# Kernel tuning notes

Measured on AMD Instinct MI355X. Metric: run time of the kernel, lower is better.

The kernel has to match this reference:

```python
import jax, jax.numpy as jnp
import numpy as np

B = 1024      # batchsz
T = 80        # max_review_len
E = 100       # embedding_len
U = 256       # units
V = 10000     # total_words


def _lstm_cell(x, c, h, wf, bf, wi, bi, wc, bc, wo, bo):
    # Faithful to LSTMlayer.call: four separate concat+matmul+bias gates.
    hx = jnp.concatenate([h, x], axis=1)          # [B, U + sec_dim]
    gf = jax.nn.sigmoid(hx @ wf + bf)             # forget gate
    gi = jax.nn.sigmoid(hx @ wi + bi)             # input gate (gr / wr1)
    ct = jnp.tanh(hx @ wc + bc)                   # candidate (wr2)
    c_new = gf * c + gi * ct
    go = jax.nn.sigmoid(hx @ wo + bo)             # output gate
    h_new = go * jnp.tanh(c_new)
    return c_new, h_new


def setup_inputs() -> dict:
    key = jax.random.key(0)
    ks = jax.random.split(key, 21)
    inp = {"tokens": jax.random.randint(ks[0], (B, T), 0, V, dtype=jnp.int32)}
    inp["emb"] = jax.random.normal(ks[1], (V, E), dtype=jnp.float32) * 0.1
    # Layer 1: sec_dim = E; Layer 2: sec_dim = U. stddev=0.1 matches init_weights.
    names = ["wf1", "wi1", "wc1", "wo1", "wf2", "wi2", "wc2", "wo2"]
    dims = [U + E] * 4 + [U + U] * 4
    for i, (n, d) in enumerate(zip(names, dims)):
        inp[n] = jax.random.normal(ks[2 + i], (d, U), dtype=jnp.float32) * 0.1
        inp["b" + n[1:]] = jnp.zeros((U,), dtype=jnp.float32)
    inp["w_out"] = jax.random.normal(ks[10], (U, 1), dtype=jnp.float32) * 0.1
    inp["b_out"] = jnp.zeros((1,), dtype=jnp.float32)
    return inp


def reference(tokens, emb, wf1, bf1, wi1, bi1, wc1, bc1, wo1, bo1,
              wf2, bf2, wi2, bi2, wc2, bc2, wo2, bo2, w_out, b_out):
    x = emb[tokens]                               # [B, T, E]
    init = (jnp.zeros((B, U), x.dtype), jnp.zeros((B, U), x.dtype),
            jnp.zeros((B, U), x.dtype), jnp.zeros((B, U), x.dtype))

    def step(carry, xt):
        c1, h1, c2, h2 = carry
        c1, h1 = _lstm_cell(xt, c1, h1, wf1, bf1, wi1, bi1, wc1, bc1, wo1, bo1)
        c2, h2 = _lstm_cell(h1, c2, h2, wf2, bf2, wi2, bi2, wc2, bc2, wo2, bo2)
        return (c1, h1, c2, h2), None

    carry, _ = jax.lax.scan(step, init, jnp.swapaxes(x, 0, 1))  # scan over T
    h2_last = carry[3]                            # [B, U]
    return jax.nn.sigmoid(h2_last @ w_out + b_out)  # [B, 1]
```

## Files before the change

### kernel.cpp

```cpp
#include <hip/hip_runtime.h>

typedef unsigned short u16;
typedef unsigned int uint;

using f32x4 = __attribute__((ext_vector_type(4))) float;
using bf16x8 = __attribute__((ext_vector_type(8))) __bf16;
using u32x4 = __attribute__((ext_vector_type(4))) uint;

static __device__ __forceinline__ bf16x8 as_bf16x8(uint4 u) {
    union { uint4 a; bf16x8 b; } c; c.a = u; return c.b;
}
static __device__ __forceinline__ bf16x8 as_bf16x8v(u32x4 u) {
    union { u32x4 a; bf16x8 b; } c; c.a = u; return c.b;
}
static __device__ __forceinline__ float bf2f(u16 h) {
    union { uint u; float f; } c; c.u = ((uint)h) << 16; return c.f;
}
static __device__ __forceinline__ u16 f2bf(float f) {
    union { float f; uint u; } c; c.f = f;
    uint u = c.u;
    return (u16)((u + 0x7fffu + ((u >> 16) & 1u)) >> 16);
}
static __device__ __forceinline__ float fast_sigmoid(float x) {
    x = fminf(30.f, fmaxf(-30.f, x));
    return __builtin_amdgcn_rcpf(1.0f + __builtin_amdgcn_exp2f(x * -1.44269504f));
}
static __device__ __forceinline__ float fast_tanh(float x) {
    x = fminf(15.f, fmaxf(-15.f, x));
    return 1.0f - 2.0f * __builtin_amdgcn_rcpf(1.0f + __builtin_amdgcn_exp2f(x * 2.88539008f));
}

static __device__ __forceinline__ u32x4 load_b128_sc0(const u16* p) {
    u32x4 r;
    asm volatile("global_load_dwordx4 %0, %1, off sc0" : "=v"(r) : "v"(p) : "memory");
    return r;
}
static __device__ __forceinline__ void wait_vm0_fence_sched() {
    asm volatile("s_waitcnt vmcnt(0)" ::: "memory");
    __builtin_amdgcn_sched_barrier(0);
}

static __device__ __forceinline__ float vext(f32x4 v, int i) {
    float r = v[0];
    r = (i == 1) ? v[1] : r;
    r = (i == 2) ? v[2] : r;
    r = (i == 3) ? v[3] : r;
    return r;
}
static __device__ __forceinline__ float sel4(float a0, float a1, float a2, float a3, int i) {
    float r = a0;
    r = (i == 1) ? a1 : r;
    r = (i == 2) ? a2 : r;
    r = (i == 3) ? a3 : r;
    return r;
}

static __device__ __forceinline__ int detect_fp32(const uint* w, int nwords) {
    int hits = 0;
    for (int i = 0; i < nwords; ++i) { uint e = (w[i] >> 7) & 0xffu; hits += (e >= 0x80u); }
    return hits > (nwords >> 3);
}
static __device__ __forceinline__ u16 load_bf(const void* p, int i, int fp32) {
    return fp32 ? f2bf(((const float*)p)[i]) : ((const u16*)p)[i];
}

__global__ void pack_w(const void* wf, const void* wi, const void* wc, const void* wo,
                       const void* bbf, const void* bbi, const void* bbc, const void* bbo,
                       u16* __restrict__ wp, u16* __restrict__ bp, int K, int KSTEPS) {
    __shared__ int sfp;
    if (threadIdx.x == 0) sfp = detect_fp32((const uint*)wf, 256);
    __syncthreads();
    const int fp32 = sfp;
    int w = blockIdx.x / KSTEPS, ks = blockIdx.x % KSTEPS;
    int nt = threadIdx.x >> 6, lane = threadIdx.x & 63;
    int c16 = lane & 15, q = lane >> 4;
    int n = w * 64 + nt * 16 + c16;
    int u = n >> 2, g = n & 3;
    const void* W = (g == 0) ? wf : (g == 1) ? wi : (g == 2) ? wc : wo;
    union { u16 v[8]; uint4 u4; } tmp;
#pragma unroll
    for (int j = 0; j < 8; ++j) {
        int k = ks * 32 + q * 8 + j;
        tmp.v[j] = (k < K) ? load_bf(W, k * 256 + u, fp32) : (u16)0;
    }
    *(uint4*)(wp + ((w * KSTEPS + ks) * 4 + nt) * 512 + lane * 8) = tmp.u4;
    if (ks == 0 && threadIdx.x < 64) {
        int n2 = w * 64 + threadIdx.x;
        int g2 = n2 & 3;
        const void* B = (g2 == 0) ? bbf : (g2 == 1) ? bbi : (g2 == 2) ? bbc : bbo;
        bp[n2] = load_bf(B, n2 >> 2, fp32);
    }
}

__global__ void pack_misc(const void* emb, const void* w_out, const void* b_out,
                          u16* __restrict__ embp, u16* __restrict__ wob,
                          u16* __restrict__ bob, uint* __restrict__ hzero) {
    __shared__ int sfp;
    if (threadIdx.x == 0) sfp = detect_fp32((const uint*)emb, 256);
    __syncthreads();
    const int fp32 = sfp;
    int gid = blockIdx.x * blockDim.x + threadIdx.x;
    int stride = gridDim.x * blockDim.x;
    for (int i = gid; i < 1000000; i += stride)
        embp[i] = load_bf(emb, i, fp32);
    for (int i = gid; i < 525312; i += stride) hzero[i] = 0;
    if (blockIdx.x == 0) {
        __shared__ int sfp2;
        if (threadIdx.x == 0) sfp2 = detect_fp32((const uint*)w_out, 128);
        __syncthreads();
        if (threadIdx.x < 256) wob[threadIdx.x] = load_bf(w_out, threadIdx.x, sfp2);
        if (threadIdx.x == 0) bob[0] = load_bf(b_out, 0, sfp2);
    }
}

static __device__ __forceinline__ void rg_arrive(uint* grp, int gself,
                                                 uint phase, int tid) {
    asm volatile("s_waitcnt vmcnt(0)" ::: "memory");
    __syncthreads();
    if (tid == 0) {
        uint* slot = grp + gself;
        asm volatile("global_store_dword %0, %1, off sc0" :: "v"(slot), "v"(phase) : "memory");
        __hip_atomic_fetch_add(grp + 32, 1u, __ATOMIC_RELAXED,
                               __HIP_MEMORY_SCOPE_AGENT);
    }
}
static __device__ __forceinline__ void rg_wait(uint* grp, uint phase, int tid) {
    if (tid < 64) {
        const uint* fp = grp + (tid & 15);
        uint* cnt = grp + 32;
        while (true) {
            uint v;
            asm volatile("global_load_dword %0, %1, off sc0\n\t"
                         "s_waitcnt vmcnt(0)"
                         : "=v"(v) : "v"(fp) : "memory");
            if (__all((int)(v >= phase))) break;
            if (__hip_atomic_load(cnt, __ATOMIC_RELAXED,
                                  __HIP_MEMORY_SCOPE_AGENT) >= 16u * phase) break;
        }
    }
    __syncthreads();
}

#define CSLAB 16384

__global__ void __launch_bounds__(1024, 1)
lstm_kernel(const int* __restrict__ tokens, const u16* __restrict__ embp,
            const u16* __restrict__ wp1, const u16* __restrict__ b1p,
            const u16* __restrict__ wp2, const u16* __restrict__ b2p,
            const u16* __restrict__ wob, const u16* __restrict__ bob,
            u16* __restrict__ h1g, u16* __restrict__ h2g,
            uint* __restrict__ flags, float* __restrict__ out) {
    __shared__ __align__(16) u16 w1s[12 * 4 * 512];
    __shared__ __align__(16) u16 w2s[16 * 4 * 512];
    __shared__ __align__(16) float outscr[1024];

    const int tid = threadIdx.x;
    const int bid = blockIdx.x;
    const int r2 = bid & 7;
    const int g = bid >> 3;
    const int lane = tid & 63;
    const int wv = tid >> 6;
    const int mt = wv >> 2, nt = wv & 3;
    const int c16 = lane & 15, q = lane >> 4;
    const int rrf = mt * 16 + c16;
    const int loff = (q >> 1) * 1024 + rrf * 16 + (q & 1) * 8;

    const int b = lane & 3;
    const int ulz = nt * 4 + ((lane & 15) >> 2);
    const int gunit = g * 16 + ulz;
    const int rloc = mt * 16 + q * 4 + b;
    const int hidx = g * 1024 + rloc * 16 + ulz;

    {
        const uint4* s1 = (const uint4*)(wp1 + g * (12 * 4 * 512));
        uint4* d1 = (uint4*)w1s;
        for (int i = tid; i < 3072; i += 1024) d1[i] = s1[i];
        const uint4* s2 = (const uint4*)(wp2 + g * (16 * 4 * 512));
        uint4* d2 = (uint4*)w2s;
        for (int i = tid; i < 4096; i += 1024) d2[i] = s2[i];
    }
    ushort4 bl1 = *(const ushort4*)(b1p + gunit * 4);
    ushort4 bl2 = *(const ushort4*)(b2p + gunit * 4);
    const float b1f = bf2f(bl1.x), b1i = bf2f(bl1.y), b1c = bf2f(bl1.z), b1o = bf2f(bl1.w);
    const float b2f = bf2f(bl2.x), b2i = bf2f(bl2.y), b2c = bf2f(bl2.z), b2o = bf2f(bl2.w);
    float c1s[2] = {0.f, 0.f}, c2s[2] = {0.f, 0.f};
    uint ph[2] = {0u, 0u};
    uint* fgrp[2] = {flags + (0 * 8 + r2) * 64, flags + (1 * 8 + r2) * 64};
    __syncthreads();

    const u16* bp1 = w1s + nt * 512 + lane * 8;
    const u16* bp2 = w2s + nt * 512 + lane * 8;

    ushort4 xlo[4], xhi[4];
#define LOAD_X(ch, t)                                                          \
    {                                                                          \
        int row = r2 * 128 + (ch) * 64 + rrf;                                  \
        int tok = tokens[row * 80 + (t)];                                      \
        const u16* xb = embp + tok * 100 + q * 8;                              \
        _Pragma("unroll")                                                      \
        for (int k2 = 0; k2 < 4; ++k2) {                                       \
            xlo[k2] = *(const ushort4*)(xb + k2 * 32);                         \
            xhi[k2] = *(const ushort4*)(xb + k2 * 32 + 4);                     \
        }                                                                      \
    }
#define XFRAG(k2) ({ union { ushort4 a[2]; bf16x8 v; } xu;                     \
                     xu.a[0] = xlo[k2]; xu.a[1] = xhi[k2]; xu.v; })

#define GATES(accv, B0, B1, B2, B3, cref, hout)                                \
    {                                                                          \
        float v0 = vext(accv, b);                                              \
        float v1 = __shfl_xor(vext(accv, b ^ 1), 1, 64);                       \
        float v2 = __shfl_xor(vext(accv, b ^ 2), 2, 64);                       \
        float v3 = __shfl_xor(vext(accv, b ^ 3), 3, 64);                       \
        float zf = sel4(v0, v1, v2, v3, b);                                    \
        float zi = sel4(v0, v1, v2, v3, b ^ 1);                                \
        float zc = sel4(v0, v1, v2, v3, b ^ 2);                                \
        float zo = sel4(v0, v1, v2, v3, b ^ 3);                                \
        float gf = fast_sigmoid(zf + B0);                                      \
        float gi = fast_sigmoid(zi + B1);                                      \
        float gc = fast_tanh(zc + B2);                                         \
        float go = fast_sigmoid(zo + B3);                                      \
        float cn = gf * cref + gi * gc;                                        \
        cref = cn;                                                             \
        hout = f2bf(go * fast_tanh(cn));                                       \
    }

#pragma unroll 1
    for (int ch = 0; ch < 2; ++ch) {
        LOAD_X(ch, 0);
        f32x4 acc = (f32x4){0.f, 0.f, 0.f, 0.f};
#pragma unroll
        for (int k2 = 0; k2 < 4; ++k2)
            acc = __builtin_amdgcn_mfma_f32_16x16x32_bf16(
                XFRAG(k2), as_bf16x8(*(const uint4*)(bp1 + (8 + k2) * 2048)), acc, 0, 0, 0);
        u16 h1o;
        GATES(acc, b1f, b1i, b1c, b1o, c1s[ch], h1o);
        h1g[((0 * 2 + ch) * 8 + r2) * CSLAB + hidx] = h1o;
        ++ph[ch];
        rg_arrive(fgrp[ch], g, ph[ch], tid);
    }

#pragma unroll 1
    for (int i = 0; i < 79; ++i) {
        const int p_h2r = (i + 1) & 1, p_h1r = i & 1;
        const int p_h2w = i & 1, p_h1w = (i + 1) & 1;
#pragma unroll 1
        for (int ch = 0; ch < 2; ++ch) {
            LOAD_X(ch, i + 1);
            rg_wait(fgrp[ch], ph[ch], tid);

            const u16* h2b = h2g + ((p_h2r * 2 + ch) * 8 + r2) * CSLAB + loff;
            const u16* h1b = h1g + ((p_h1r * 2 + ch) * 8 + r2) * CSLAB + loff;
            u32x4 ag[16];
#pragma unroll
            for (int ks = 0; ks < 8; ++ks) ag[ks] = load_b128_sc0(h2b + ks * 2048);
#pragma unroll
            for (int ks = 0; ks < 8; ++ks) ag[8 + ks] = load_b128_sc0(h1b + ks * 2048);
            wait_vm0_fence_sched();

            f32x4 acc2 = (f32x4){0.f, 0.f, 0.f, 0.f};
#pragma unroll
            for (int ks = 0; ks < 16; ++ks)
                acc2 = __builtin_amdgcn_mfma_f32_16x16x32_bf16(
                    as_bf16x8v(ag[ks]), as_bf16x8(*(const uint4*)(bp2 + ks * 2048)), acc2, 0, 0, 0);
            f32x4 acc1 = (f32x4){0.f, 0.f, 0.f, 0.f};
#pragma unroll
            for (int ks = 0; ks < 8; ++ks)
                acc1 = __builtin_amdgcn_mfma_f32_16x16x32_bf16(
                    as_bf16x8v(ag[8 + ks]), as_bf16x8(*(const uint4*)(bp1 + ks * 2048)), acc1, 0, 0, 0);
#pragma unroll
            for (int k2 = 0; k2 < 4; ++k2)
                acc1 = __builtin_amdgcn_mfma_f32_16x16x32_bf16(
                    XFRAG(k2), as_bf16x8(*(const uint4*)(bp1 + (8 + k2) * 2048)), acc1, 0, 0, 0);

            u16 h2o, h1o;
            GATES(acc2, b2f, b2i, b2c, b2o, c2s[ch], h2o);
            GATES(acc1, b1f, b1i, b1c, b1o, c1s[ch], h1o);
            h2g[((p_h2w * 2 + ch) * 8 + r2) * CSLAB + hidx] = h2o;
            h1g[((p_h1w * 2 + ch) * 8 + r2) * CSLAB + hidx] = h1o;

            ++ph[ch];
            rg_arrive(fgrp[ch], g, ph[ch], tid);
        }
    }

#pragma unroll 1
    for (int ch = 0; ch < 2; ++ch) {
        rg_wait(fgrp[ch], ph[ch], tid);
        const u16* h2b = h2g + ((0 * 2 + ch) * 8 + r2) * CSLAB + loff;
        const u16* h1b = h1g + ((1 * 2 + ch) * 8 + r2) * CSLAB + loff;
        u32x4 ag[16];
#pragma unroll
        for (int ks = 0; ks < 8; ++ks) ag[ks] = load_b128_sc0(h2b + ks * 2048);
#pragma unroll
        for (int ks = 0; ks < 8; ++ks) ag[8 + ks] = load_b128_sc0(h1b + ks * 2048);
        wait_vm0_fence_sched();
        f32x4 acc2 = (f32x4){0.f, 0.f, 0.f, 0.f};
#pragma unroll
        for (int ks = 0; ks < 16; ++ks)
            acc2 = __builtin_amdgcn_mfma_f32_16x16x32_bf16(
                as_bf16x8v(ag[ks]), as_bf16x8(*(const uint4*)(bp2 + ks * 2048)), acc2, 0, 0, 0);
        u16 h2o;
        GATES(acc2, b2f, b2i, b2c, b2o, c2s[ch], h2o);
        h2g[((1 * 2 + ch) * 8 + r2) * CSLAB + hidx] = h2o;
        ++ph[ch];
        rg_arrive(fgrp[ch], g, ph[ch], tid);
    }
    rg_wait(fgrp[0], ph[0], tid);
    rg_wait(fgrp[1], ph[1], tid);

    if (g == 0) {
#pragma unroll 1
        for (int ch = 0; ch < 2; ++ch) {
            const u16* base = h2g + ((1 * 2 + ch) * 8 + r2) * CSLAB;
            int rr = tid >> 4, s = tid & 15;
            const u16* hp = base + s * 1024 + rr * 16;
            u32x4 hv0 = load_b128_sc0(hp);
            u32x4 hv1 = load_b128_sc0(hp + 8);
            wait_vm0_fence_sched();
            const u16* wq = wob + s * 16;
            union { u32x4 v[2]; u16 h[16]; } hu; hu.v[0] = hv0; hu.v[1] = hv1;
            float dot = 0.f;
#pragma unroll
            for (int k = 0; k < 16; ++k) dot += bf2f(hu.h[k]) * bf2f(wq[k]);
            __syncthreads();
            outscr[rr * 16 + s] = dot;
            __syncthreads();
            if (tid < 64) {
                float ssum = 0.f;
                for (int k = 0; k < 16; ++k) ssum += outscr[tid * 16 + k];
                out[r2 * 128 + ch * 64 + tid] = fast_sigmoid(ssum + bf2f(bob[0]));
            }
        }
    }
}

extern "C" void kernel_launch(void* const* d_in, const int* in_sizes, int n_in,
                              void* d_out, int out_size, void* d_ws, size_t ws_size,
                              hipStream_t stream) {
    const int* tokens = (const int*)d_in[0];
    const void* emb = d_in[1];
    const void* wf1 = d_in[2];  const void* bf1_ = d_in[3];
    const void* wi1 = d_in[4];  const void* bi1_ = d_in[5];
    const void* wc1 = d_in[6];  const void* bc1_ = d_in[7];
    const void* wo1 = d_in[8];  const void* bo1_ = d_in[9];
    const void* wf2 = d_in[10]; const void* bf2_ = d_in[11];
    const void* wi2 = d_in[12]; const void* bi2_ = d_in[13];
    const void* wc2 = d_in[14]; const void* bc2_ = d_in[15];
    const void* wo2 = d_in[16]; const void* bo2_ = d_in[17];
    const void* w_out = d_in[18];
    const void* b_out = d_in[19];

    u16* wp1 = (u16*)d_ws;
    u16* wp2 = wp1 + 16 * 12 * 4 * 512;
    u16* b1p = wp2 + 16 * 16 * 4 * 512;
    u16* b2p = b1p + 1024;
    u16* wob = b2p + 1024;
    u16* bob = wob + 256;
    u16* embp = bob + 8;
    u16* h1g = embp + 1000000;
    u16* h2g = h1g + 524288;
    uint* flags = (uint*)(h2g + 524288);

    pack_w<<<dim3(16 * 12), dim3(256), 0, stream>>>(wf1, wi1, wc1, wo1, bf1_, bi1_, bc1_, bo1_,
                                                    wp1, b1p, 356, 12);
    pack_w<<<dim3(16 * 16), dim3(256), 0, stream>>>(wf2, wi2, wc2, wo2, bf2_, bi2_, bc2_, bo2_,
                                                    wp2, b2p, 512, 16);
    pack_misc<<<dim3(512), dim3(256), 0, stream>>>(emb, w_out, b_out, embp, wob, bob, (uint*)h1g);
    lstm_kernel<<<dim3(128), dim3(1024), 0, stream>>>(tokens, embp, wp1, b1p, wp2, b2p,
                                                      wob, bob, h1g, h2g, flags, (float*)d_out);
}
```

Before: 885.6 us.

## Unskew LSTM layers with separate h1/h2 flags and staged coalesced publishes

```diff
diff --git a/kernel.cpp b/kernel.cpp
--- a/kernel.cpp
+++ b/kernel.cpp
@@ -103,7 +103,7 @@
     int stride = gridDim.x * blockDim.x;
     for (int i = gid; i < 1000000; i += stride)
         embp[i] = load_bf(emb, i, fp32);
-    for (int i = gid; i < 525312; i += stride) hzero[i] = 0;
+    for (int i = gid; i < 526336; i += stride) hzero[i] = 0;
     if (blockIdx.x == 0) {
         __shared__ int sfp2;
         if (threadIdx.x == 0) sfp2 = detect_fp32((const uint*)w_out, 128);
@@ -113,33 +113,44 @@
     }
 }
 
-static __device__ __forceinline__ void rg_arrive(uint* grp, int gself,
-                                                 uint phase, int tid) {
-    asm volatile("s_waitcnt vmcnt(0)" ::: "memory");
-    __syncthreads();
-    if (tid == 0) {
-        uint* slot = grp + gself;
-        asm volatile("global_store_dword %0, %1, off sc0" :: "v"(slot), "v"(phase) : "memory");
-        __hip_atomic_fetch_add(grp + 32, 1u, __ATOMIC_RELAXED,
-                               __HIP_MEMORY_SCOPE_AGENT);
-    }
-}
 static __device__ __forceinline__ void rg_wait(uint* grp, uint phase, int tid) {
     if (tid < 64) {
         const uint* fp = grp + (tid & 15);
         uint* cnt = grp + 32;
+        int k = 0;
         while (true) {
             uint v;
             asm volatile("global_load_dword %0, %1, off sc0\n\t"
                          "s_waitcnt vmcnt(0)"
                          : "=v"(v) : "v"(fp) : "memory");
             if (__all((int)(v >= phase))) break;
-            if (__hip_atomic_load(cnt, __ATOMIC_RELAXED,
-                                  __HIP_MEMORY_SCOPE_AGENT) >= 16u * phase) break;
+            if (((++k) & 7) == 0 &&
+                __hip_atomic_load(cnt, __ATOMIC_RELAXED,
+                                  __HIP_MEMORY_SCOPE_AGENT) >= 16u * phase)
+                break;
         }
     }
     __syncthreads();
 }
+
+#define PUBLISH(stg, dstbase, grp, phval)                                      \
+    __syncthreads();                                                           \
+    if (tid < 64) {                                                            \
+        const uint4* s4 = (const uint4*)(stg);                                 \
+        uint4 v0 = s4[lane * 2], v1 = s4[lane * 2 + 1];                        \
+        u16* dp = (dstbase) + g * 1024 + lane * 16;                            \
+        *(uint4*)dp = v0;                                                      \
+        *(uint4*)(dp + 8) = v1;                                                \
+        asm volatile("s_waitcnt vmcnt(0)" ::: "memory");                       \
+        if (tid == 0) {                                                        \
+            uint* slot = (grp) + g;                                            \
+            uint pv = (phval);                                                 \
+            asm volatile("global_store_dword %0, %1, off sc0"                  \
+                         :: "v"(slot), "v"(pv) : "memory");                    \
+            __hip_atomic_fetch_add((grp) + 32, 1u, __ATOMIC_RELAXED,           \
+                                   __HIP_MEMORY_SCOPE_AGENT);                  \
+        }                                                                      \
+    }
 
 #define CSLAB 16384
 
@@ -152,6 +163,8 @@
             uint* __restrict__ flags, float* __restrict__ out) {
     __shared__ __align__(16) u16 w1s[12 * 4 * 512];
     __shared__ __align__(16) u16 w2s[16 * 4 * 512];
+    __shared__ __align__(16) u16 stg1[1024];
+    __shared__ __align__(16) u16 stg2[1024];
     __shared__ __align__(16) float outscr[1024];
 
     const int tid = threadIdx.x;
@@ -169,7 +182,7 @@
     const int ulz = nt * 4 + ((lane & 15) >> 2);
     const int gunit = g * 16 + ulz;
     const int rloc = mt * 16 + q * 4 + b;
-    const int hidx = g * 1024 + rloc * 16 + ulz;
+    const int hlin = rloc * 16 + ulz;
 
     {
         const uint4* s1 = (const uint4*)(wp1 + g * (12 * 4 * 512));
@@ -184,8 +197,8 @@
     const float b1f = bf2f(bl1.x), b1i = bf2f(bl1.y), b1c = bf2f(bl1.z), b1o = bf2f(bl1.w);
     const float b2f = bf2f(bl2.x), b2i = bf2f(bl2.y), b2c = bf2f(bl2.z), b2o = bf2f(bl2.w);
     float c1s[2] = {0.f, 0.f}, c2s[2] = {0.f, 0.f};
-    uint ph[2] = {0u, 0u};
-    uint* fgrp[2] = {flags + (0 * 8 + r2) * 64, flags + (1 * 8 + r2) * 64};
+    uint* f1g[2] = {flags + ((0 * 2 + 0) * 8 + r2) * 64, flags + ((0 * 2 + 1) * 8 + r2) * 64};
+    uint* f2g[2] = {flags + ((1 * 2 + 0) * 8 + r2) * 64, flags + ((1 * 2 + 1) * 8 + r2) * 64};
     __syncthreads();
 
     const u16* bp1 = w1s + nt * 512 + lane * 8;
@@ -225,19 +238,29 @@
         hout = f2bf(go * fast_tanh(cn));                                       \
     }
 
-#pragma unroll 1
-    for (int ch = 0; ch < 2; ++ch) {
-        LOAD_X(ch, 0);
+    {
+        LOAD_X(0, 0);
         f32x4 acc = (f32x4){0.f, 0.f, 0.f, 0.f};
 #pragma unroll
         for (int k2 = 0; k2 < 4; ++k2)
             acc = __builtin_amdgcn_mfma_f32_16x16x32_bf16(
                 XFRAG(k2), as_bf16x8(*(const uint4*)(bp1 + (8 + k2) * 2048)), acc, 0, 0, 0);
         u16 h1o;
-        GATES(acc, b1f, b1i, b1c, b1o, c1s[ch], h1o);
-        h1g[((0 * 2 + ch) * 8 + r2) * CSLAB + hidx] = h1o;
-        ++ph[ch];
-        rg_arrive(fgrp[ch], g, ph[ch], tid);
+        GATES(acc, b1f, b1i, b1c, b1o, c1s[0], h1o);
+        stg1[hlin] = h1o;
+        PUBLISH(stg1, h1g + ((0 * 2 + 0) * 8 + r2) * CSLAB, f1g[0], 1u);
+    }
+    {
+        LOAD_X(1, 0);
+        f32x4 acc = (f32x4){0.f, 0.f, 0.f, 0.f};
+#pragma unroll
+        for (int k2 = 0; k2 < 4; ++k2)
+            acc = __builtin_amdgcn_mfma_f32_16x16x32_bf16(
+                XFRAG(k2), as_bf16x8(*(const uint4*)(bp1 + (8 + k2) * 2048)), acc, 0, 0, 0);
+        u16 h1o;
+        GATES(acc, b1f, b1i, b1c, b1o, c1s[1], h1o);
+        stg2[hlin] = h1o;
+        PUBLISH(stg2, h1g + ((0 * 2 + 1) * 8 + r2) * CSLAB, f1g[1], 1u);
     }
 
 #pragma unroll 1
@@ -247,67 +270,81 @@
 #pragma unroll 1
         for (int ch = 0; ch < 2; ++ch) {
             LOAD_X(ch, i + 1);
-            rg_wait(fgrp[ch], ph[ch], tid);
-
-            const u16* h2b = h2g + ((p_h2r * 2 + ch) * 8 + r2) * CSLAB + loff;
-            const u16* h1b = h1g + ((p_h1r * 2 + ch) * 8 + r2) * CSLAB + loff;
-            u32x4 ag[16];
-#pragma unroll
-            for (int ks = 0; ks < 8; ++ks) ag[ks] = load_b128_sc0(h2b + ks * 2048);
-#pragma unroll
-            for (int ks = 0; ks < 8; ++ks) ag[8 + ks] = load_b128_sc0(h1b + ks * 2048);
-            wait_vm0_fence_sched();
-
-            f32x4 acc2 = (f32x4){0.f, 0.f, 0.f, 0.f};
-#pragma unroll
-            for (int ks = 0; ks < 16; ++ks)
-                acc2 = __builtin_amdgcn_mfma_f32_16x16x32_bf16(
-                    as_bf16x8v(ag[ks]), as_bf16x8(*(const uint4*)(bp2 + ks * 2048)), acc2, 0, 0, 0);
             f32x4 acc1 = (f32x4){0.f, 0.f, 0.f, 0.f};
-#pragma unroll
-            for (int ks = 0; ks < 8; ++ks)
-                acc1 = __builtin_amdgcn_mfma_f32_16x16x32_bf16(
-                    as_bf16x8v(ag[8 + ks]), as_bf16x8(*(const uint4*)(bp1 + ks * 2048)), acc1, 0, 0, 0);
 #pragma unroll
             for (int k2 = 0; k2 < 4; ++k2)
                 acc1 = __builtin_amdgcn_mfma_f32_16x16x32_bf16(
                     XFRAG(k2), as_bf16x8(*(const uint4*)(bp1 + (8 + k2) * 2048)), acc1, 0, 0, 0);
 
-            u16 h2o, h1o;
+            if (i) rg_wait(f2g[ch], (uint)i, tid);
+            const u16* h2b = h2g + ((p_h2r * 2 + ch) * 8 + r2) * CSLAB + loff;
+            u32x4 ag2[8];
+#pragma unroll
+            for (int ks = 0; ks < 8; ++ks) ag2[ks] = load_b128_sc0(h2b + ks * 2048);
+            wait_vm0_fence_sched();
+            f32x4 acc2 = (f32x4){0.f, 0.f, 0.f, 0.f};
+#pragma unroll
+            for (int ks = 0; ks < 8; ++ks)
+                acc2 = __builtin_amdgcn_mfma_f32_16x16x32_bf16(
+                    as_bf16x8v(ag2[ks]), as_bf16x8(*(const uint4*)(bp2 + ks * 2048)), acc2, 0, 0, 0);
+
+            rg_wait(f1g[ch], (uint)(i + 1), tid);
+            const u16* h1b = h1g + ((p_h1r * 2 + ch) * 8 + r2) * CSLAB + loff;
+            u32x4 ag1[8];
+#pragma unroll
+            for (int ks = 0; ks < 8; ++ks) ag1[ks] = load_b128_sc0(h1b + ks * 2048);
+            wait_vm0_fence_sched();
+
+#pragma unroll
+            for (int ks = 0; ks < 8; ++ks)
+                acc1 = __builtin_amdgcn_mfma_f32_16x16x32_bf16(
+                    as_bf16x8v(ag1[ks]), as_bf16x8(*(const uint4*)(bp1 + ks * 2048)), acc1, 0, 0, 0);
+            u16 h1o;
+            GATES(acc1, b1f, b1i, b1c, b1o, c1s[ch], h1o);
+            stg1[hlin] = h1o;
+            PUBLISH(stg1, h1g + ((p_h1w * 2 + ch) * 8 + r2) * CSLAB, f1g[ch], (uint)(i + 2));
+
+#pragma unroll
+            for (int ks = 0; ks < 8; ++ks)
+                acc2 = __builtin_amdgcn_mfma_f32_16x16x32_bf16(
+                    as_bf16x8v(ag1[ks]), as_bf16x8(*(const uint4*)(bp2 + (8 + ks) * 2048)), acc2, 0, 0, 0);
+            u16 h2o;
             GATES(acc2, b2f, b2i, b2c, b2o, c2s[ch], h2o);
-            GATES(acc1, b1f, b1i, b1c, b1o, c1s[ch], h1o);
-            h2g[((p_h2w * 2 + ch) * 8 + r2) * CSLAB + hidx] = h2o;
-            h1g[((p_h1w * 2 + ch) * 8 + r2) * CSLAB + hidx] = h1o;
-
-            ++ph[ch];
-            rg_arrive(fgrp[ch], g, ph[ch], tid);
+            stg2[hlin] = h2o;
+            PUBLISH(stg2, h2g + ((p_h2w * 2 + ch) * 8 + r2) * CSLAB, f2g[ch], (uint)(i + 1));
         }
     }
 
 #pragma unroll 1
     for (int ch = 0; ch < 2; ++ch) {
-        rg_wait(fgrp[ch], ph[ch], tid);
+        rg_wait(f2g[ch], 79u, tid);
         const u16* h2b = h2g + ((0 * 2 + ch) * 8 + r2) * CSLAB + loff;
-        const u16* h1b = h1g + ((1 * 2 + ch) * 8 + r2) * CSLAB + loff;
-        u32x4 ag[16];
-#pragma unroll
-        for (int ks = 0; ks < 8; ++ks) ag[ks] = load_b128_sc0(h2b + ks * 2048);
-#pragma unroll
-        for (int ks = 0; ks < 8; ++ks) ag[8 + ks] = load_b128_sc0(h1b + ks * 2048);
+        u32x4 ag2[8];
+#pragma unroll
+        for (int ks = 0; ks < 8; ++ks) ag2[ks] = load_b128_sc0(h2b + ks * 2048);
         wait_vm0_fence_sched();
         f32x4 acc2 = (f32x4){0.f, 0.f, 0.f, 0.f};
 #pragma unroll
-        for (int ks = 0; ks < 16; ++ks)
+        for (int ks = 0; ks < 8; ++ks)
             acc2 = __builtin_amdgcn_mfma_f32_16x16x32_bf16(
-                as_bf16x8v(ag[ks]), as_bf16x8(*(const uint4*)(bp2 + ks * 2048)), acc2, 0, 0, 0);
+                as_bf16x8v(ag2[ks]), as_bf16x8(*(const uint4*)(bp2 + ks * 2048)), acc2, 0, 0, 0);
+        rg_wait(f1g[ch], 80u, tid);
+        const u16* h1b = h1g + ((1 * 2 + ch) * 8 + r2) * CSLAB + loff;
+        u32x4 ag1[8];
+#pragma unroll
+        for (int ks = 0; ks < 8; ++ks) ag1[ks] = load_b128_sc0(h1b + ks * 2048);
+        wait_vm0_fence_sched();
+#pragma unroll
+        for (int ks = 0; ks < 8; ++ks)
+            acc2 = __builtin_amdgcn_mfma_f32_16x16x32_bf16(
+                as_bf16x8v(ag1[ks]), as_bf16x8(*(const uint4*)(bp2 + (8 + ks) * 2048)), acc2, 0, 0, 0);
         u16 h2o;
         GATES(acc2, b2f, b2i, b2c, b2o, c2s[ch], h2o);
-        h2g[((1 * 2 + ch) * 8 + r2) * CSLAB + hidx] = h2o;
-        ++ph[ch];
-        rg_arrive(fgrp[ch], g, ph[ch], tid);
-    }
-    rg_wait(fgrp[0], ph[0], tid);
-    rg_wait(fgrp[1], ph[1], tid);
+        stg2[hlin] = h2o;
+        PUBLISH(stg2, h2g + ((1 * 2 + ch) * 8 + r2) * CSLAB, f2g[ch], 80u);
+    }
+    rg_wait(f2g[0], 80u, tid);
+    rg_wait(f2g[1], 80u, tid);
 
     if (g == 0) {
 #pragma unroll 1
```

After: 949.1 us. +7.2%, slower.

## Split batch into four 32-row chunks with 512-thread blocks and overlap x-MFMA before wait

Applied to the files above, without the earlier changes.

```diff
diff --git a/kernel.cpp b/kernel.cpp
--- a/kernel.cpp
+++ b/kernel.cpp
@@ -103,7 +103,7 @@
     int stride = gridDim.x * blockDim.x;
     for (int i = gid; i < 1000000; i += stride)
         embp[i] = load_bf(emb, i, fp32);
-    for (int i = gid; i < 525312; i += stride) hzero[i] = 0;
+    for (int i = gid; i < 526336; i += stride) hzero[i] = 0;
     if (blockIdx.x == 0) {
         __shared__ int sfp2;
         if (threadIdx.x == 0) sfp2 = detect_fp32((const uint*)w_out, 128);
@@ -113,37 +113,41 @@
     }
 }
 
-static __device__ __forceinline__ void rg_arrive(uint* grp, int gself,
-                                                 uint phase, int tid) {
-    asm volatile("s_waitcnt vmcnt(0)" ::: "memory");
-    __syncthreads();
-    if (tid == 0) {
-        uint* slot = grp + gself;
-        asm volatile("global_store_dword %0, %1, off sc0" :: "v"(slot), "v"(phase) : "memory");
-        __hip_atomic_fetch_add(grp + 32, 1u, __ATOMIC_RELAXED,
-                               __HIP_MEMORY_SCOPE_AGENT);
-    }
-}
 static __device__ __forceinline__ void rg_wait(uint* grp, uint phase, int tid) {
     if (tid < 64) {
         const uint* fp = grp + (tid & 15);
         uint* cnt = grp + 32;
+        int k = 0;
         while (true) {
             uint v;
             asm volatile("global_load_dword %0, %1, off sc0\n\t"
                          "s_waitcnt vmcnt(0)"
                          : "=v"(v) : "v"(fp) : "memory");
             if (__all((int)(v >= phase))) break;
-            if (__hip_atomic_load(cnt, __ATOMIC_RELAXED,
-                                  __HIP_MEMORY_SCOPE_AGENT) >= 16u * phase) break;
+            if (((++k) & 7) == 0 &&
+                __hip_atomic_load(cnt, __ATOMIC_RELAXED,
+                                  __HIP_MEMORY_SCOPE_AGENT) >= 16u * phase)
+                break;
         }
     }
     __syncthreads();
 }
 
-#define CSLAB 16384
-
-__global__ void __launch_bounds__(1024, 1)
+static __device__ __forceinline__ void rg_arrive(uint* grp, int gself,
+                                                 uint phase, int tid) {
+    asm volatile("s_waitcnt vmcnt(0)" ::: "memory");
+    __syncthreads();
+    if (tid == 0) {
+        uint* slot = grp + gself;
+        asm volatile("global_store_dword %0, %1, off sc0" :: "v"(slot), "v"(phase) : "memory");
+        __hip_atomic_fetch_add(grp + 32, 1u, __ATOMIC_RELAXED,
+                               __HIP_MEMORY_SCOPE_AGENT);
+    }
+}
+
+#define CSLAB 8192
+
+__global__ void __launch_bounds__(512, 1)
 lstm_kernel(const int* __restrict__ tokens, const u16* __restrict__ embp,
             const u16* __restrict__ wp1, const u16* __restrict__ b1p,
             const u16* __restrict__ wp2, const u16* __restrict__ b2p,
@@ -152,7 +156,7 @@
             uint* __restrict__ flags, float* __restrict__ out) {
     __shared__ __align__(16) u16 w1s[12 * 4 * 512];
     __shared__ __align__(16) u16 w2s[16 * 4 * 512];
-    __shared__ __align__(16) float outscr[1024];
+    __shared__ __align__(16) float outscr[512];
 
     const int tid = threadIdx.x;
     const int bid = blockIdx.x;
@@ -163,29 +167,30 @@
     const int mt = wv >> 2, nt = wv & 3;
     const int c16 = lane & 15, q = lane >> 4;
     const int rrf = mt * 16 + c16;
-    const int loff = (q >> 1) * 1024 + rrf * 16 + (q & 1) * 8;
+    const int loff = (q >> 1) * 512 + rrf * 16 + (q & 1) * 8;
 
     const int b = lane & 3;
     const int ulz = nt * 4 + ((lane & 15) >> 2);
     const int gunit = g * 16 + ulz;
     const int rloc = mt * 16 + q * 4 + b;
-    const int hidx = g * 1024 + rloc * 16 + ulz;
+    const int hidx = g * 512 + rloc * 16 + ulz;
 
     {
         const uint4* s1 = (const uint4*)(wp1 + g * (12 * 4 * 512));
         uint4* d1 = (uint4*)w1s;
-        for (int i = tid; i < 3072; i += 1024) d1[i] = s1[i];
+        for (int i = tid; i < 3072; i += 512) d1[i] = s1[i];
         const uint4* s2 = (const uint4*)(wp2 + g * (16 * 4 * 512));
         uint4* d2 = (uint4*)w2s;
-        for (int i = tid; i < 4096; i += 1024) d2[i] = s2[i];
+        for (int i = tid; i < 4096; i += 512) d2[i] = s2[i];
     }
     ushort4 bl1 = *(const ushort4*)(b1p + gunit * 4);
     ushort4 bl2 = *(const ushort4*)(b2p + gunit * 4);
     const float b1f = bf2f(bl1.x), b1i = bf2f(bl1.y), b1c = bf2f(bl1.z), b1o = bf2f(bl1.w);
     const float b2f = bf2f(bl2.x), b2i = bf2f(bl2.y), b2c = bf2f(bl2.z), b2o = bf2f(bl2.w);
-    float c1s[2] = {0.f, 0.f}, c2s[2] = {0.f, 0.f};
-    uint ph[2] = {0u, 0u};
-    uint* fgrp[2] = {flags + (0 * 8 + r2) * 64, flags + (1 * 8 + r2) * 64};
+    float c1s[4] = {0.f, 0.f, 0.f, 0.f}, c2s[4] = {0.f, 0.f, 0.f, 0.f};
+    uint* fg[4];
+#pragma unroll
+    for (int ch = 0; ch < 4; ++ch) fg[ch] = flags + (ch * 8 + r2) * 64;
     __syncthreads();
 
     const u16* bp1 = w1s + nt * 512 + lane * 8;
@@ -194,7 +199,7 @@
     ushort4 xlo[4], xhi[4];
 #define LOAD_X(ch, t)                                                          \
     {                                                                          \
-        int row = r2 * 128 + (ch) * 64 + rrf;                                  \
+        int row = r2 * 128 + (ch) * 32 + rrf;                                  \
         int tok = tokens[row * 80 + (t)];                                      \
         const u16* xb = embp + tok * 100 + q * 8;                              \
         _Pragma("unroll")                                                      \
@@ -225,8 +230,8 @@
         hout = f2bf(go * fast_tanh(cn));                                       \
     }
 
-#pragma unroll 1
-    for (int ch = 0; ch < 2; ++ch) {
+#pragma unroll
+    for (int ch = 0; ch < 4; ++ch) {
         LOAD_X(ch, 0);
         f32x4 acc = (f32x4){0.f, 0.f, 0.f, 0.f};
 #pragma unroll
@@ -235,86 +240,92 @@
                 XFRAG(k2), as_bf16x8(*(const uint4*)(bp1 + (8 + k2) * 2048)), acc, 0, 0, 0);
         u16 h1o;
         GATES(acc, b1f, b1i, b1c, b1o, c1s[ch], h1o);
-        h1g[((0 * 2 + ch) * 8 + r2) * CSLAB + hidx] = h1o;
-        ++ph[ch];
-        rg_arrive(fgrp[ch], g, ph[ch], tid);
+        h1g[((0 * 4 + ch) * 8 + r2) * CSLAB + hidx] = h1o;
+        rg_arrive(fg[ch], g, 1u, tid);
     }
 
 #pragma unroll 1
     for (int i = 0; i < 79; ++i) {
         const int p_h2r = (i + 1) & 1, p_h1r = i & 1;
         const int p_h2w = i & 1, p_h1w = (i + 1) & 1;
-#pragma unroll 1
-        for (int ch = 0; ch < 2; ++ch) {
+#pragma unroll
+        for (int ch = 0; ch < 4; ++ch) {
             LOAD_X(ch, i + 1);
-            rg_wait(fgrp[ch], ph[ch], tid);
-
-            const u16* h2b = h2g + ((p_h2r * 2 + ch) * 8 + r2) * CSLAB + loff;
-            const u16* h1b = h1g + ((p_h1r * 2 + ch) * 8 + r2) * CSLAB + loff;
-            u32x4 ag[16];
-#pragma unroll
-            for (int ks = 0; ks < 8; ++ks) ag[ks] = load_b128_sc0(h2b + ks * 2048);
-#pragma unroll
-            for (int ks = 0; ks < 8; ++ks) ag[8 + ks] = load_b128_sc0(h1b + ks * 2048);
-            wait_vm0_fence_sched();
-
-            f32x4 acc2 = (f32x4){0.f, 0.f, 0.f, 0.f};
-#pragma unroll
-            for (int ks = 0; ks < 16; ++ks)
-                acc2 = __builtin_amdgcn_mfma_f32_16x16x32_bf16(
-                    as_bf16x8v(ag[ks]), as_bf16x8(*(const uint4*)(bp2 + ks * 2048)), acc2, 0, 0, 0);
             f32x4 acc1 = (f32x4){0.f, 0.f, 0.f, 0.f};
-#pragma unroll
-            for (int ks = 0; ks < 8; ++ks)
-                acc1 = __builtin_amdgcn_mfma_f32_16x16x32_bf16(
-                    as_bf16x8v(ag[8 + ks]), as_bf16x8(*(const uint4*)(bp1 + ks * 2048)), acc1, 0, 0, 0);
 #pragma unroll
             for (int k2 = 0; k2 < 4; ++k2)
                 acc1 = __builtin_amdgcn_mfma_f32_16x16x32_bf16(
                     XFRAG(k2), as_bf16x8(*(const uint4*)(bp1 + (8 + k2) * 2048)), acc1, 0, 0, 0);
 
+            rg_wait(fg[ch], (uint)(i + 1), tid);
+
+            const u16* h2b = h2g + ((p_h2r * 4 + ch) * 8 + r2) * CSLAB + loff;
+            const u16* h1b = h1g + ((p_h1r * 4 + ch) * 8 + r2) * CSLAB + loff;
+            u32x4 ag2[8], ag1[8];
+#pragma unroll
+            for (int ks = 0; ks < 8; ++ks) ag2[ks] = load_b128_sc0(h2b + ks * 1024);
+#pragma unroll
+            for (int ks = 0; ks < 8; ++ks) ag1[ks] = load_b128_sc0(h1b + ks * 1024);
+            wait_vm0_fence_sched();
+
+            f32x4 acc2 = (f32x4){0.f, 0.f, 0.f, 0.f};
+#pragma unroll
+            for (int ks = 0; ks < 8; ++ks)
+                acc2 = __builtin_amdgcn_mfma_f32_16x16x32_bf16(
+                    as_bf16x8v(ag2[ks]), as_bf16x8(*(const uint4*)(bp2 + ks * 2048)), acc2, 0, 0, 0);
+#pragma unroll
+            for (int ks = 0; ks < 8; ++ks)
+                acc2 = __builtin_amdgcn_mfma_f32_16x16x32_bf16(
+                    as_bf16x8v(ag1[ks]), as_bf16x8(*(const uint4*)(bp2 + (8 + ks) * 2048)), acc2, 0, 0, 0);
+#pragma unroll
+            for (int ks = 0; ks < 8; ++ks)
+                acc1 = __builtin_amdgcn_mfma_f32_16x16x32_bf16(
+                    as_bf16x8v(ag1[ks]), as_bf16x8(*(const uint4*)(bp1 + ks * 2048)), acc1, 0, 0, 0);
+
             u16 h2o, h1o;
             GATES(acc2, b2f, b2i, b2c, b2o, c2s[ch], h2o);
             GATES(acc1, b1f, b1i, b1c, b1o, c1s[ch], h1o);
-            h2g[((p_h2w * 2 + ch) * 8 + r2) * CSLAB + hidx] = h2o;
-            h1g[((p_h1w * 2 + ch) * 8 + r2) * CSLAB + hidx] = h1o;
-
-            ++ph[ch];
-            rg_arrive(fgrp[ch], g, ph[ch], tid);
+            h2g[((p_h2w * 4 + ch) * 8 + r2) * CSLAB + hidx] = h2o;
+            h1g[((p_h1w * 4 + ch) * 8 + r2) * CSLAB + hidx] = h1o;
+
+            rg_arrive(fg[ch], g, (uint)(i + 2), tid);
         }
     }
 
-#pragma unroll 1
-    for (int ch = 0; ch < 2; ++ch) {
-        rg_wait(fgrp[ch], ph[ch], tid);
-        const u16* h2b = h2g + ((0 * 2 + ch) * 8 + r2) * CSLAB + loff;
-        const u16* h1b = h1g + ((1 * 2 + ch) * 8 + r2) * CSLAB + loff;
-        u32x4 ag[16];
-#pragma unroll
-        for (int ks = 0; ks < 8; ++ks) ag[ks] = load_b128_sc0(h2b + ks * 2048);
-#pragma unroll
-        for (int ks = 0; ks < 8; ++ks) ag[8 + ks] = load_b128_sc0(h1b + ks * 2048);
+#pragma unroll
+    for (int ch = 0; ch < 4; ++ch) {
+        rg_wait(fg[ch], 80u, tid);
+        const u16* h2b = h2g + ((0 * 4 + ch) * 8 + r2) * CSLAB + loff;
+        const u16* h1b = h1g + ((1 * 4 + ch) * 8 + r2) * CSLAB + loff;
+        u32x4 ag2[8], ag1[8];
+#pragma unroll
+        for (int ks = 0; ks < 8; ++ks) ag2[ks] = load_b128_sc0(h2b + ks * 1024);
+#pragma unroll
+        for (int ks = 0; ks < 8; ++ks) ag1[ks] = load_b128_sc0(h1b + ks * 1024);
         wait_vm0_fence_sched();
         f32x4 acc2 = (f32x4){0.f, 0.f, 0.f, 0.f};
 #pragma unroll
-        for (int ks = 0; ks < 16; ++ks)
+        for (int ks = 0; ks < 8; ++ks)
             acc2 = __builtin_amdgcn_mfma_f32_16x16x32_bf16(
-                as_bf16x8v(ag[ks]), as_bf16x8(*(const uint4*)(bp2 + ks * 2048)), acc2, 0, 0, 0);
+                as_bf16x8v(ag2[ks]), as_bf16x8(*(const uint4*)(bp2 + ks * 2048)), acc2, 0, 0, 0);
+#pragma unroll
+        for (int ks = 0; ks < 8; ++ks)
+            acc2 = __builtin_amdgcn_mfma_f32_16x16x32_bf16(
+                as_bf16x8v(ag1[ks]), as_bf16x8(*(const uint4*)(bp2 + (8 + ks) * 2048)), acc2, 0, 0, 0);
         u16 h2o;
         GATES(acc2, b2f, b2i, b2c, b2o, c2s[ch], h2o);
-        h2g[((1 * 2 + ch) * 8 + r2) * CSLAB + hidx] = h2o;
-        ++ph[ch];
-        rg_arrive(fgrp[ch], g, ph[ch], tid);
-    }
-    rg_wait(fgrp[0], ph[0], tid);
-    rg_wait(fgrp[1], ph[1], tid);
+        h2g[((1 * 4 + ch) * 8 + r2) * CSLAB + hidx] = h2o;
+        rg_arrive(fg[ch], g, 81u, tid);
+    }
+#pragma unroll
+    for (int ch = 0; ch < 4; ++ch) rg_wait(fg[ch], 81u, tid);
 
     if (g == 0) {
 #pragma unroll 1
-        for (int ch = 0; ch < 2; ++ch) {
-            const u16* base = h2g + ((1 * 2 + ch) * 8 + r2) * CSLAB;
+        for (int ch = 0; ch < 4; ++ch) {
+            const u16* base = h2g + ((1 * 4 + ch) * 8 + r2) * CSLAB;
             int rr = tid >> 4, s = tid & 15;
-            const u16* hp = base + s * 1024 + rr * 16;
+            const u16* hp = base + s * 512 + rr * 16;
             u32x4 hv0 = load_b128_sc0(hp);
             u32x4 hv1 = load_b128_sc0(hp + 8);
             wait_vm0_fence_sched();
@@ -326,10 +337,10 @@
             __syncthreads();
             outscr[rr * 16 + s] = dot;
             __syncthreads();
-            if (tid < 64) {
+            if (tid < 32) {
                 float ssum = 0.f;
                 for (int k = 0; k < 16; ++k) ssum += outscr[tid * 16 + k];
-                out[r2 * 128 + ch * 64 + tid] = fast_sigmoid(ssum + bf2f(bob[0]));
+                out[r2 * 128 + ch * 32 + tid] = fast_sigmoid(ssum + bf2f(bob[0]));
             }
         }
     }
@@ -367,6 +378,6 @@
     pack_w<<<dim3(16 * 16), dim3(256), 0, stream>>>(wf2, wi2, wc2, wo2, bf2_, bi2_, bc2_, bo2_,
                                                     wp2, b2p, 512, 16);
     pack_misc<<<dim3(512), dim3(256), 0, stream>>>(emb, w_out, b_out, embp, wob, bob, (uint*)h1g);
-    lstm_kernel<<<dim3(128), dim3(1024), 0, stream>>>(tokens, embp, wp1, b1p, wp2, b2p,
-                                                      wob, bob, h1g, h2g, flags, (float*)d_out);
-}
+    lstm_kernel<<<dim3(128), dim3(512), 0, stream>>>(tokens, embp, wp1, b1p, wp2, b2p,
+                                                     wob, bob, h1g, h2g, flags, (float*)d_out);
+}
```

After: 1.053 ms. +18.9%, slower.

## Split block into two independent half-groups with per-wave grid barrier arrivals

Applied to the files above, without the earlier changes.

```diff
diff --git a/kernel.cpp b/kernel.cpp
--- a/kernel.cpp
+++ b/kernel.cpp
@@ -103,7 +103,7 @@
     int stride = gridDim.x * blockDim.x;
     for (int i = gid; i < 1000000; i += stride)
         embp[i] = load_bf(emb, i, fp32);
-    for (int i = gid; i < 525312; i += stride) hzero[i] = 0;
+    for (int i = gid; i < 526336; i += stride) hzero[i] = 0;
     if (blockIdx.x == 0) {
         __shared__ int sfp2;
         if (threadIdx.x == 0) sfp2 = detect_fp32((const uint*)w_out, 128);
@@ -113,32 +113,37 @@
     }
 }
 
-static __device__ __forceinline__ void rg_arrive(uint* grp, int gself,
-                                                 uint phase, int tid) {
+static __device__ __forceinline__ void wv_wait(uint* grp, uint phase, int lane) {
+    const uint* fp = grp + (lane & 15);
+    uint* cnt = grp + 32;
+    int k = 0;
+    while (true) {
+        uint v;
+        asm volatile("global_load_dword %0, %1, off sc0\n\t"
+                     "s_waitcnt vmcnt(0)"
+                     : "=v"(v) : "v"(fp) : "memory");
+        if (__all((int)(v >= phase))) break;
+        if (((++k) & 7) == 0 &&
+            __hip_atomic_load(cnt, __ATOMIC_RELAXED,
+                              __HIP_MEMORY_SCOPE_AGENT) >= 16u * phase)
+            break;
+    }
+}
+
+static __device__ __forceinline__ void wv_arrive(uint* ldsc_ch, uint* grp, int g,
+                                                 uint phase, int lane) {
     asm volatile("s_waitcnt vmcnt(0)" ::: "memory");
-    __syncthreads();
-    if (tid == 0) {
-        uint* slot = grp + gself;
-        asm volatile("global_store_dword %0, %1, off sc0" :: "v"(slot), "v"(phase) : "memory");
-        __hip_atomic_fetch_add(grp + 32, 1u, __ATOMIC_RELAXED,
-                               __HIP_MEMORY_SCOPE_AGENT);
-    }
-}
-static __device__ __forceinline__ void rg_wait(uint* grp, uint phase, int tid) {
-    if (tid < 64) {
-        const uint* fp = grp + (tid & 15);
-        uint* cnt = grp + 32;
-        while (true) {
-            uint v;
-            asm volatile("global_load_dword %0, %1, off sc0\n\t"
-                         "s_waitcnt vmcnt(0)"
-                         : "=v"(v) : "v"(fp) : "memory");
-            if (__all((int)(v >= phase))) break;
-            if (__hip_atomic_load(cnt, __ATOMIC_RELAXED,
-                                  __HIP_MEMORY_SCOPE_AGENT) >= 16u * phase) break;
+    if (lane == 0) {
+        uint old = __hip_atomic_fetch_add(ldsc_ch, 1u, __ATOMIC_RELAXED,
+                                          __HIP_MEMORY_SCOPE_WORKGROUP);
+        if (old == 8u * phase - 1u) {
+            uint* slot = grp + g;
+            asm volatile("global_store_dword %0, %1, off sc0"
+                         :: "v"(slot), "v"(phase) : "memory");
+            __hip_atomic_fetch_add(grp + 32, 1u, __ATOMIC_RELAXED,
+                                   __HIP_MEMORY_SCOPE_AGENT);
         }
     }
-    __syncthreads();
 }
 
 #define CSLAB 16384
@@ -152,6 +157,7 @@
             uint* __restrict__ flags, float* __restrict__ out) {
     __shared__ __align__(16) u16 w1s[12 * 4 * 512];
     __shared__ __align__(16) u16 w2s[16 * 4 * 512];
+    __shared__ uint ldsc[2];
     __shared__ __align__(16) float outscr[1024];
 
     const int tid = threadIdx.x;
@@ -160,16 +166,15 @@
     const int g = bid >> 3;
     const int lane = tid & 63;
     const int wv = tid >> 6;
-    const int mt = wv >> 2, nt = wv & 3;
+    const int half = wv >> 3;
+    const int w8 = wv & 7;
+    const int nt = w8 & 3;
+    const int mb = (w8 >> 2) * 2;
     const int c16 = lane & 15, q = lane >> 4;
-    const int rrf = mt * 16 + c16;
-    const int loff = (q >> 1) * 1024 + rrf * 16 + (q & 1) * 8;
 
     const int b = lane & 3;
     const int ulz = nt * 4 + ((lane & 15) >> 2);
     const int gunit = g * 16 + ulz;
-    const int rloc = mt * 16 + q * 4 + b;
-    const int hidx = g * 1024 + rloc * 16 + ulz;
 
     {
         const uint4* s1 = (const uint4*)(wp1 + g * (12 * 4 * 512));
@@ -178,23 +183,24 @@
         const uint4* s2 = (const uint4*)(wp2 + g * (16 * 4 * 512));
         uint4* d2 = (uint4*)w2s;
         for (int i = tid; i < 4096; i += 1024) d2[i] = s2[i];
+        if (tid < 2) ldsc[tid] = 0u;
     }
     ushort4 bl1 = *(const ushort4*)(b1p + gunit * 4);
     ushort4 bl2 = *(const ushort4*)(b2p + gunit * 4);
     const float b1f = bf2f(bl1.x), b1i = bf2f(bl1.y), b1c = bf2f(bl1.z), b1o = bf2f(bl1.w);
     const float b2f = bf2f(bl2.x), b2i = bf2f(bl2.y), b2c = bf2f(bl2.z), b2o = bf2f(bl2.w);
-    float c1s[2] = {0.f, 0.f}, c2s[2] = {0.f, 0.f};
-    uint ph[2] = {0u, 0u};
-    uint* fgrp[2] = {flags + (0 * 8 + r2) * 64, flags + (1 * 8 + r2) * 64};
+    float c1a = 0.f, c1b = 0.f, c2a = 0.f, c2b = 0.f;
+    uint* fg = flags + (half * 8 + r2) * 64;
+    uint* lc = &ldsc[half];
     __syncthreads();
 
     const u16* bp1 = w1s + nt * 512 + lane * 8;
     const u16* bp2 = w2s + nt * 512 + lane * 8;
 
     ushort4 xlo[4], xhi[4];
-#define LOAD_X(ch, t)                                                          \
+#define LOAD_X(m, t)                                                           \
     {                                                                          \
-        int row = r2 * 128 + (ch) * 64 + rrf;                                  \
+        int row = r2 * 128 + half * 64 + (m) * 16 + c16;                       \
         int tok = tokens[row * 80 + (t)];                                      \
         const u16* xb = embp + tok * 100 + q * 8;                              \
         _Pragma("unroll")                                                      \
@@ -225,89 +231,120 @@
         hout = f2bf(go * fast_tanh(cn));                                       \
     }
 
-#pragma unroll 1
-    for (int ch = 0; ch < 2; ++ch) {
-        LOAD_X(ch, 0);
+#define MSUB(m, acc1, c1ref, c2ref, p2r, p1r, p2w, p1w, iw)                    \
+    {                                                                          \
+        const int loffm = (q >> 1) * 1024 + ((m) * 16 + c16) * 16 + (q & 1) * 8; \
+        const int hidxm = g * 1024 + ((m) * 16 + q * 4 + b) * 16 + ulz;        \
+        const u16* h2b = h2g + (((p2r) * 2 + half) * 8 + r2) * CSLAB + loffm;  \
+        const u16* h1b = h1g + (((p1r) * 2 + half) * 8 + r2) * CSLAB + loffm;  \
+        u32x4 ag2[8], ag1[8];                                                  \
+        _Pragma("unroll")                                                      \
+        for (int ks = 0; ks < 8; ++ks) ag2[ks] = load_b128_sc0(h2b + ks * 2048); \
+        _Pragma("unroll")                                                      \
+        for (int ks = 0; ks < 8; ++ks) ag1[ks] = load_b128_sc0(h1b + ks * 2048); \
+        wait_vm0_fence_sched();                                                \
+        f32x4 acc2 = (f32x4){0.f, 0.f, 0.f, 0.f};                              \
+        _Pragma("unroll")                                                      \
+        for (int ks = 0; ks < 8; ++ks)                                         \
+            acc2 = __builtin_amdgcn_mfma_f32_16x16x32_bf16(                    \
+                as_bf16x8v(ag2[ks]), as_bf16x8(*(const uint4*)(bp2 + ks * 2048)), acc2, 0, 0, 0); \
+        _Pragma("unroll")                                                      \
+        for (int ks = 0; ks < 8; ++ks)                                         \
+            acc2 = __builtin_amdgcn_mfma_f32_16x16x32_bf16(                    \
+                as_bf16x8v(ag1[ks]), as_bf16x8(*(const uint4*)(bp2 + (8 + ks) * 2048)), acc2, 0, 0, 0); \
+        _Pragma("unroll")                                                      \
+        for (int ks = 0; ks < 8; ++ks)                                         \
+            acc1 = __builtin_amdgcn_mfma_f32_16x16x32_bf16(                    \
+                as_bf16x8v(ag1[ks]), as_bf16x8(*(const uint4*)(bp1 + ks * 2048)), acc1, 0, 0, 0); \
+        u16 h2o, h1o;                                                          \
+        GATES(acc2, b2f, b2i, b2c, b2o, c2ref, h2o);                           \
+        GATES(acc1, b1f, b1i, b1c, b1o, c1ref, h1o);                           \
+        h2g[(((p2w) * 2 + half) * 8 + r2) * CSLAB + hidxm] = h2o;              \
+        h1g[(((p1w) * 2 + half) * 8 + r2) * CSLAB + hidxm] = h1o;              \
+        (void)(iw);                                                            \
+    }
+
+    {
+        LOAD_X(mb, 0);
         f32x4 acc = (f32x4){0.f, 0.f, 0.f, 0.f};
 #pragma unroll
         for (int k2 = 0; k2 < 4; ++k2)
             acc = __builtin_amdgcn_mfma_f32_16x16x32_bf16(
                 XFRAG(k2), as_bf16x8(*(const uint4*)(bp1 + (8 + k2) * 2048)), acc, 0, 0, 0);
         u16 h1o;
-        GATES(acc, b1f, b1i, b1c, b1o, c1s[ch], h1o);
-        h1g[((0 * 2 + ch) * 8 + r2) * CSLAB + hidx] = h1o;
-        ++ph[ch];
-        rg_arrive(fgrp[ch], g, ph[ch], tid);
+        GATES(acc, b1f, b1i, b1c, b1o, c1a, h1o);
+        h1g[((0 * 2 + half) * 8 + r2) * CSLAB + g * 1024 + (mb * 16 + q * 4 + b) * 16 + ulz] = h1o;
+        LOAD_X(mb + 1, 0);
+        f32x4 accB = (f32x4){0.f, 0.f, 0.f, 0.f};
+#pragma unroll
+        for (int k2 = 0; k2 < 4; ++k2)
+            accB = __builtin_amdgcn_mfma_f32_16x16x32_bf16(
+                XFRAG(k2), as_bf16x8(*(const uint4*)(bp1 + (8 + k2) * 2048)), accB, 0, 0, 0);
+        u16 h1oB;
+        GATES(accB, b1f, b1i, b1c, b1o, c1b, h1oB);
+        h1g[((0 * 2 + half) * 8 + r2) * CSLAB + g * 1024 + ((mb + 1) * 16 + q * 4 + b) * 16 + ulz] = h1oB;
+        wv_arrive(lc, fg, g, 1u, lane);
     }
 
 #pragma unroll 1
     for (int i = 0; i < 79; ++i) {
         const int p_h2r = (i + 1) & 1, p_h1r = i & 1;
         const int p_h2w = i & 1, p_h1w = (i + 1) & 1;
+
+        LOAD_X(mb, i + 1);
+        f32x4 acc1a = (f32x4){0.f, 0.f, 0.f, 0.f};
+#pragma unroll
+        for (int k2 = 0; k2 < 4; ++k2)
+            acc1a = __builtin_amdgcn_mfma_f32_16x16x32_bf16(
+                XFRAG(k2), as_bf16x8(*(const uint4*)(bp1 + (8 + k2) * 2048)), acc1a, 0, 0, 0);
+        LOAD_X(mb + 1, i + 1);
+        f32x4 acc1b = (f32x4){0.f, 0.f, 0.f, 0.f};
+#pragma unroll
+        for (int k2 = 0; k2 < 4; ++k2)
+            acc1b = __builtin_amdgcn_mfma_f32_16x16x32_bf16(
+                XFRAG(k2), as_bf16x8(*(const uint4*)(bp1 + (8 + k2) * 2048)), acc1b, 0, 0, 0);
+
+        wv_wait(fg, (uint)(i + 1), lane);
+
+        MSUB(mb, acc1a, c1a, c2a, p_h2r, p_h1r, p_h2w, p_h1w, i);
+        MSUB(mb + 1, acc1b, c1b, c2b, p_h2r, p_h1r, p_h2w, p_h1w, i);
+
+        wv_arrive(lc, fg, g, (uint)(i + 2), lane);
+    }
+
+    {
+        wv_wait(fg, 80u, lane);
 #pragma unroll 1
-        for (int ch = 0; ch < 2; ++ch) {
-            LOAD_X(ch, i + 1);
-            rg_wait(fgrp[ch], ph[ch], tid);
-
-            const u16* h2b = h2g + ((p_h2r * 2 + ch) * 8 + r2) * CSLAB + loff;
-            const u16* h1b = h1g + ((p_h1r * 2 + ch) * 8 + r2) * CSLAB + loff;
-            u32x4 ag[16];
-#pragma unroll
-            for (int ks = 0; ks < 8; ++ks) ag[ks] = load_b128_sc0(h2b + ks * 2048);
-#pragma unroll
-            for (int ks = 0; ks < 8; ++ks) ag[8 + ks] = load_b128_sc0(h1b + ks * 2048);
+        for (int s = 0; s < 2; ++s) {
+            const int m = mb + s;
+            const int loffm = (q >> 1) * 1024 + (m * 16 + c16) * 16 + (q & 1) * 8;
+            const int hidxm = g * 1024 + (m * 16 + q * 4 + b) * 16 + ulz;
+            const u16* h2b = h2g + ((0 * 2 + half) * 8 + r2) * CSLAB + loffm;
+            const u16* h1b = h1g + ((1 * 2 + half) * 8 + r2) * CSLAB + loffm;
+            u32x4 ag2[8], ag1[8];
+#pragma unroll
+            for (int ks = 0; ks < 8; ++ks) ag2[ks] = load_b128_sc0(h2b + ks * 2048);
+#pragma unroll
+            for (int ks = 0; ks < 8; ++ks) ag1[ks] = load_b128_sc0(h1b + ks * 2048);
             wait_vm0_fence_sched();
-
             f32x4 acc2 = (f32x4){0.f, 0.f, 0.f, 0.f};
 #pragma unroll
-            for (int ks = 0; ks < 16; ++ks)
+            for (int ks = 0; ks < 8; ++ks)
                 acc2 = __builtin_amdgcn_mfma_f32_16x16x32_bf16(
-                    as_bf16x8v(ag[ks]), as_bf16x8(*(const uint4*)(bp2 + ks * 2048)), acc2, 0, 0, 0);
-            f32x4 acc1 = (f32x4){0.f, 0.f, 0.f, 0.f};
+                    as_bf16x8v(ag2[ks]), as_bf16x8(*(const uint4*)(bp2 + ks * 2048)), acc2, 0, 0, 0);
 #pragma unroll
             for (int ks = 0; ks < 8; ++ks)
-                acc1 = __builtin_amdgcn_mfma_f32_16x16x32_bf16(
-                    as_bf16x8v(ag[8 + ks]), as_bf16x8(*(const uint4*)(bp1 + ks * 2048)), acc1, 0, 0, 0);
-#pragma unroll
-            for (int k2 = 0; k2 < 4; ++k2)
-                acc1 = __builtin_amdgcn_mfma_f32_16x16x32_bf16(
-                    XFRAG(k2), as_bf16x8(*(const uint4*)(bp1 + (8 + k2) * 2048)), acc1, 0, 0, 0);
-
-            u16 h2o, h1o;
-            GATES(acc2, b2f, b2i, b2c, b2o, c2s[ch], h2o);
-            GATES(acc1, b1f, b1i, b1c, b1o, c1s[ch], h1o);
-            h2g[((p_h2w * 2 + ch) * 8 + r2) * CSLAB + hidx] = h2o;
-            h1g[((p_h1w * 2 + ch) * 8 + r2) * CSLAB + hidx] = h1o;
-
-            ++ph[ch];
-            rg_arrive(fgrp[ch], g, ph[ch], tid);
+                acc2 = __builtin_amdgcn_mfma_f32_16x16x32_bf16(
+                    as_bf16x8v(ag1[ks]), as_bf16x8(*(const uint4*)(bp2 + (8 + ks) * 2048)), acc2, 0, 0, 0);
+            u16 h2o;
+            if (s == 0) { GATES(acc2, b2f, b2i, b2c, b2o, c2a, h2o); }
+            else        { GATES(acc2, b2f, b2i, b2c, b2o, c2b, h2o); }
+            h2g[((1 * 2 + half) * 8 + r2) * CSLAB + hidxm] = h2o;
         }
-    }
-
-#pragma unroll 1
-    for (int ch = 0; ch < 2; ++ch) {
-        rg_wait(fgrp[ch], ph[ch], tid);
-        const u16* h2b = h2g + ((0 * 2 + ch) * 8 + r2) * CSLAB + loff;
-        const u16* h1b = h1g + ((1 * 2 + ch) * 8 + r2) * CSLAB + loff;
-        u32x4 ag[16];
-#pragma unroll
-        for (int ks = 0; ks < 8; ++ks) ag[ks] = load_b128_sc0(h2b + ks * 2048);
-#pragma unroll
-        for (int ks = 0; ks < 8; ++ks) ag[8 + ks] = load_b128_sc0(h1b + ks * 2048);
-        wait_vm0_fence_sched();
-        f32x4 acc2 = (f32x4){0.f, 0.f, 0.f, 0.f};
-#pragma unroll
-        for (int ks = 0; ks < 16; ++ks)
-            acc2 = __builtin_amdgcn_mfma_f32_16x16x32_bf16(
-                as_bf16x8v(ag[ks]), as_bf16x8(*(const uint4*)(bp2 + ks * 2048)), acc2, 0, 0, 0);
-        u16 h2o;
-        GATES(acc2, b2f, b2i, b2c, b2o, c2s[ch], h2o);
-        h2g[((1 * 2 + ch) * 8 + r2) * CSLAB + hidx] = h2o;
-        ++ph[ch];
-        rg_arrive(fgrp[ch], g, ph[ch], tid);
-    }
-    rg_wait(fgrp[0], ph[0], tid);
-    rg_wait(fgrp[1], ph[1], tid);
+        wv_arrive(lc, fg, g, 81u, lane);
+        wv_wait(fg, 81u, lane);
+    }
+    __syncthreads();
 
     if (g == 0) {
 #pragma unroll 1
```

Result: faster. 836.7 us (-5.5%).
